# Optimization experiments

Hardware: AMD Instinct MI355X
Metric: run time of the kernel (lower is better)

The kernel has to match this reference:

```python
import jax, jax.numpy as jnp
from jax import lax
import numpy as np

# ---- geometry constants (from metadata / module __init__) ----
NA = 1152            # rotview (number of projection angles)
ND = 736             # det_count
NP = 512             # reconstructed image size
VOX = 1.0 / 0.7      # vox_scaling
D   = VOX * 595.0    # source-to-isocenter distance
DD  = VOX * 490.6    # isocenter-to-detector distance
DU  = VOX * 1.2858   # detector pixel spacing
DSD = D + DD         # source-to-detector distance
ANGLES = np.linspace(0.0, 2.0 * np.pi, NA, endpoint=False) + np.pi / 2.0

# ---- Shepp-Logan Fourier filter (skimage/torch-radon construction) ----
PAD = max(64, int(2 ** np.ceil(np.log2(2 * ND))))  # 2048

def _shepp_logan_filter(size):
    n = np.concatenate([np.arange(1, size // 2 + 1, 2),
                        np.arange(size // 2 - 1, 0, -2)])
    f = np.zeros(size)
    f[0] = 0.25
    f[1::2] = -1.0 / (np.pi * n) ** 2
    four = 2.0 * np.real(np.fft.fft(f))            # ramp filter
    omega = np.pi * np.fft.fftfreq(size)[1:]
    four[1:] *= np.sin(omega) / omega              # Shepp-Logan window
    return four[: size // 2 + 1].astype(np.float32)  # rfft half-spectrum

FILT = jnp.asarray(_shepp_logan_filter(PAD))
COS_A = jnp.asarray(np.cos(ANGLES).astype(np.float32))
SIN_A = jnp.asarray(np.sin(ANGLES).astype(np.float32))


def _filter_sinogram(sino):
    # sino: (NA, ND). Zero-pad to PAD, filter in Fourier domain, crop.
    padded = jnp.pad(sino, ((0, 0), (0, PAD - ND)))
    spec = jnp.fft.rfft(padded, axis=-1) * FILT
    filt = jnp.fft.irfft(spec, n=PAD, axis=-1)[:, :ND]
    return filt * (np.pi / (2.0 * NA))


def _backproject(filtered):
    # Pixel-driven fan-beam (flat detector) backprojection.
    c = (NP - 1) / 2.0
    coords = jnp.arange(NP, dtype=jnp.float32) - c
    ys, xs = jnp.meshgrid(coords, coords, indexing='ij')  # (NP, NP)

    def body(acc, inp):
        cb, sb, row = inp
        pdot = xs * cb + ys * sb            # pixel coord along source dir
        pe = -xs * sb + ys * cb             # pixel coord along detector axis
        den = D - pdot                      # source->pixel depth
        u = DSD * pe / den                  # detector coordinate (mm)
        iu = u / DU + (ND - 1) / 2.0        # fractional detector index
        i0 = jnp.floor(iu)
        frac = iu - i0
        i0i = i0.astype(jnp.int32)
        valid = (i0i >= 0) & (i0i < ND - 1) & (den > 0)
        i0c = jnp.clip(i0i, 0, ND - 2)
        v = row[i0c] * (1.0 - frac) + row[i0c + 1] * frac  # linear interp
        w = (D / den) ** 2                   # fan-beam distance weighting
        return acc + jnp.where(valid, w * v, 0.0), None

    img, _ = lax.scan(body, jnp.zeros((NP, NP), jnp.float32),
                      (COS_A, SIN_A, filtered))
    return img


def setup_inputs() -> dict:
    key = jax.random.key(0)
    x = jax.random.normal(key, (1, 1, NA, ND), dtype=jnp.float32)
    return {"x": x}


def reference(x):
    sino = x[0, 0]                          # (NA, ND) after squeeze
    filtered = _filter_sinogram(sino)
    fbp = _backproject(filtered)
    # mu -> HU -> normalize to [0, 1] window
    fbp_hu = (1000.0 * ((fbp - 0.0192) / 0.0192) - (-1024.0)) / (3072.0 - (-1024.0))
    return fbp_hu[None, None]               # (1, 1, 512, 512)
```

## Files before the change

kernel.cpp:

```cpp
#include <hip/hip_runtime.h>
#include <math.h>

#ifndef M_PI
#define M_PI 3.14159265358979323846
#endif

#define NAANG 1152
#define NDET  736
#define NPIX  512
#define PADN  2048
#define NHALF 1025

#define OFF_COST  0
#define OFF_FILTF 8192
#define OFF_H     12416
#define OFF_TRIG  20608
#define OFF_FS    39040
#define OFF_PART  3430528

typedef int int32x4_t __attribute__((ext_vector_type(4)));
__device__ float llvm_amdgcn_struct_buffer_load_fp32(int32x4_t srsrc,
                                                     int vindex, int voffset,
                                                     int soffset, int cachepolicy)
    __asm("llvm.amdgcn.struct.buffer.load.f32");

__global__ void costab_kernel(float* __restrict__ cosT) {
    int r = blockIdx.x * 256 + threadIdx.x;
    cosT[r] = (float)cos(2.0 * M_PI * (double)r / (double)PADN);
}

__global__ void filt_spec_kernel(const float* __restrict__ cosT,
                                 float* __restrict__ filt_f) {
    __shared__ float red[256];
    const int m = blockIdx.x;
    const int t = threadIdx.x;
    float s = 0.f;
    for (int j = t; j < 1024; j += 256) {
        int n = (j < 512) ? (2 * j + 1) : (2047 - 2 * j);
        float fj = (float)(-1.0 / ((M_PI * n) * (M_PI * n)));
        s += fj * cosT[(m * (2 * j + 1)) & (PADN - 1)];
    }
    red[t] = s;
    __syncthreads();
    for (int w = 128; w > 0; w >>= 1) {
        if (t < w) red[t] += red[t + w];
        __syncthreads();
    }
    if (t == 0) {
        double four = 2.0 * (0.25 + (double)red[0]);
        if (m > 0) {
            double om = M_PI * (double)m / (double)PADN;
            four *= sin(om) / om;
        }
        filt_f[m] = (float)four;
    }
}

__global__ void h_kernel(const float* __restrict__ cosT,
                         const float* __restrict__ filt_f,
                         float* __restrict__ h, float4* __restrict__ trig) {
    __shared__ float red[256];
    const int k = blockIdx.x;
    const int t = threadIdx.x;
    if (t == 0 && k < NAANG) {
        double ang = 2.0 * M_PI * (double)k / (double)NAANG + M_PI / 2.0;
        double c = cos(ang), s = sin(ang);
        double K = 1085.6 / 1.2858;
        trig[k] = make_float4((float)c, (float)s, (float)(K * c), (float)(K * s));
    }
    float s = 0.f;
    for (int m = t; m <= 1024; m += 256) {
        float F = filt_f[m];
        float c;
        if (m == 0) c = 1.f;
        else if (m == 1024) c = (k & 1) ? -1.f : 1.f;
        else c = 2.f * cosT[(m * k) & (PADN - 1)];
        s += F * c;
    }
    red[t] = s;
    __syncthreads();
    for (int w = 128; w > 0; w >>= 1) {
        if (t < w) red[t] += red[t + w];
        __syncthreads();
    }
    if (t == 0)
        h[k] = (float)((double)red[0] / (double)PADN * (M_PI / (2.0 * (double)NAANG)));
}

__global__ void conv_kernel(const float* __restrict__ x,
                            const float* __restrict__ h,
                            float* __restrict__ fs) {
    __shared__ float sh2[2816];
    __shared__ float srow[NDET];
    const int row = blockIdx.x;
    const int t = threadIdx.x;
    const float4* h4 = (const float4*)h;
    for (int i = t; i < 704; i += 192) ((float4*)sh2)[i] = h4[i & 511];
    const float4* x4 = (const float4*)(x + row * NDET);
    for (int i = t; i < NDET / 4; i += 192) ((float4*)srow)[i] = x4[i];
    __syncthreads();

    const int t4 = 4 * t;
    float o0 = 0.f, o1 = 0.f, o2 = 0.f, o3 = 0.f;
    #pragma unroll 2
    for (int j = 0; j < NDET; j += 4) {
        float4 r4 = *(const float4*)&srow[j];
        const int A = t4 + PADN - j;
        float4 hlo = *(const float4*)&sh2[A - 4];
        float4 hhi = *(const float4*)&sh2[A];
        o0 = fmaf(r4.x, hhi.x, o0); o0 = fmaf(r4.y, hlo.w, o0);
        o0 = fmaf(r4.z, hlo.z, o0); o0 = fmaf(r4.w, hlo.y, o0);
        o1 = fmaf(r4.x, hhi.y, o1); o1 = fmaf(r4.y, hhi.x, o1);
        o1 = fmaf(r4.z, hlo.w, o1); o1 = fmaf(r4.w, hlo.z, o1);
        o2 = fmaf(r4.x, hhi.z, o2); o2 = fmaf(r4.y, hhi.y, o2);
        o2 = fmaf(r4.z, hhi.x, o2); o2 = fmaf(r4.w, hlo.w, o2);
        o3 = fmaf(r4.x, hhi.w, o3); o3 = fmaf(r4.y, hhi.z, o3);
        o3 = fmaf(r4.z, hhi.y, o3); o3 = fmaf(r4.w, hhi.x, o3);
    }
    if (t < NDET / 4)
        *(float4*)&fs[row * NDET + t4] = make_float4(o0, o1, o2, o3);
}

#define GEO(AA, S)                                                       \
  {                                                                      \
    float4 q = trig[abase + (AA)];           \
    const float* rp_ = fs + (size_t)(abase + (AA)) * NDET;               \
    uintptr_t ua_ = (uintptr_t)rp_;                                      \
    int32x4_t sA_ = { (int)ua_, (int)(ua_ >> 32) | 0x00040000, 735,      \
                      0x00020000 };                                      \
    uintptr_t ub_ = ua_ + 4;                                             \
    int32x4_t sB_ = { (int)ub_, (int)(ub_ >> 32) | 0x00040000, 735,      \
                      0x00020000 };                                      \
    float den0 = fmaf(-xs, q.x, fmaf(-ys0, q.y, Dg));                    \
    float kpe0 = fmaf(ys0, q.z, -(xs * q.w));                            \
    float den1 = den0 - q.y, den2 = den1 - q.y, den3 = den2 - q.y;       \
    float kpe1 = kpe0 + q.z, kpe2 = kpe1 + q.z, kpe3 = kpe2 + q.z;       \
    float r0 = __builtin_amdgcn_rcpf(den0);                              \
    float r1 = __builtin_amdgcn_rcpf(den1);                              \
    float r2 = __builtin_amdgcn_rcpf(den2);                              \
    float r3 = __builtin_amdgcn_rcpf(den3);                              \
    float iu0 = fmaf(kpe0, r0, 367.5f);                                  \
    float iu1 = fmaf(kpe1, r1, 367.5f);                                  \
    float iu2 = fmaf(kpe2, r2, 367.5f);                                  \
    float iu3 = fmaf(kpe3, r3, 367.5f);                                  \
    int i0 = (int)floorf(iu0);                                           \
    int i1 = (int)floorf(iu1);                                           \
    int i2 = (int)floorf(iu2);                                           \
    int i3 = (int)floorf(iu3);                                           \
    asm("v_fract_f32 %0, %1" : "=v"(S##f0) : "v"(iu0));                  \
    asm("v_fract_f32 %0, %1" : "=v"(S##f1) : "v"(iu1));                  \
    asm("v_fract_f32 %0, %1" : "=v"(S##f2) : "v"(iu2));                  \
    asm("v_fract_f32 %0, %1" : "=v"(S##f3) : "v"(iu3));                  \
    S##g0l = llvm_amdgcn_struct_buffer_load_fp32(sA_, i0, 0, 0, 0);      \
    S##g0h = llvm_amdgcn_struct_buffer_load_fp32(sB_, i0, 0, 0, 0);      \
    S##g1l = llvm_amdgcn_struct_buffer_load_fp32(sA_, i1, 0, 0, 0);      \
    S##g1h = llvm_amdgcn_struct_buffer_load_fp32(sB_, i1, 0, 0, 0);      \
    S##g2l = llvm_amdgcn_struct_buffer_load_fp32(sA_, i2, 0, 0, 0);      \
    S##g2h = llvm_amdgcn_struct_buffer_load_fp32(sB_, i2, 0, 0, 0);      \
    S##g3l = llvm_amdgcn_struct_buffer_load_fp32(sA_, i3, 0, 0, 0);      \
    S##g3h = llvm_amdgcn_struct_buffer_load_fp32(sB_, i3, 0, 0, 0);      \
    S##w0 = r0 * r0; S##w1 = r1 * r1; S##w2 = r2 * r2; S##w3 = r3 * r3;  \
  }

#define CONSUME(S)                                                       \
  {                                                                      \
    float v0 = fmaf(S##f0, S##g0h - S##g0l, S##g0l);                     \
    float v1 = fmaf(S##f1, S##g1h - S##g1l, S##g1l);                     \
    float v2 = fmaf(S##f2, S##g2h - S##g2l, S##g2l);                     \
    float v3 = fmaf(S##f3, S##g3h - S##g3l, S##g3l);                     \
    acc0 = fmaf(S##w0, v0, acc0); acc1 = fmaf(S##w1, v1, acc1);          \
    acc2 = fmaf(S##w2, v2, acc2); acc3 = fmaf(S##w3, v3, acc3);          \
  }

#define DECLSET(S)                                                       \
    float S##g0l, S##g0h, S##g1l, S##g1h, S##g2l, S##g2h, S##g3l, S##g3h;\
    float S##f0, S##f1, S##f2, S##f3, S##w0, S##w1, S##w2, S##w3;

template<int NCH>
__global__ __launch_bounds__(256, 6)
void backproj_kernel(const float* __restrict__ fs,
                     const float4* __restrict__ trig,
                     float* __restrict__ partial) {
    constexpr int ACL = NAANG / NCH;
    static_assert(ACL % 3 == 0, "pipeline tail assumes ACL divisible by 3");
    const int t = threadIdx.x;
    const int abase = blockIdx.z * ACL;
    const int ix = blockIdx.x * 256 + t;
    const int iy = blockIdx.y * 4;
    const float xs  = (float)ix - 255.5f;
    const float ys0 = (float)iy - 255.5f;
    const float Dg = 850.0f;

    float acc0 = 0.f, acc1 = 0.f, acc2 = 0.f, acc3 = 0.f;
    DECLSET(A) DECLSET(B) DECLSET(C)

    GEO(0, A);
    GEO(1, B);
    int a = 0;
    for (; a + 5 < ACL; a += 3) {
        GEO(a + 2, C); CONSUME(A);
        GEO(a + 3, A); CONSUME(B);
        GEO(a + 4, B); CONSUME(C);
    }
    GEO(a + 2, C);
    CONSUME(A); CONSUME(B); CONSUME(C);

    float* outp = partial + ((size_t)blockIdx.z * NPIX + iy) * NPIX + ix;
    outp[0 * NPIX] = acc0;
    outp[1 * NPIX] = acc1;
    outp[2 * NPIX] = acc2;
    outp[3 * NPIX] = acc3;
}

template<int NCH>
__global__ void combine_kernel(const float* __restrict__ partial,
                               float* __restrict__ out) {
    int p = blockIdx.x * 256 + threadIdx.x;
    float s = 0.f;
    #pragma unroll
    for (int c = 0; c < NCH; ++c) s += partial[c * NPIX * NPIX + p];
    out[p] = fmaf(s, (float)(722500.0 * 1000.0 / 0.0192 / 4096.0), 0.005859375f);
}

extern "C" void kernel_launch(void* const* d_in, const int* in_sizes, int n_in,
                              void* d_out, int out_size, void* d_ws, size_t ws_size,
                              hipStream_t stream) {
    const float* x = (const float*)d_in[0];
    float* out = (float*)d_out;

    char* ws = (char*)d_ws;
    float*  cosT   = (float*)(ws + OFF_COST);
    float*  filt_f = (float*)(ws + OFF_FILTF);
    float*  h      = (float*)(ws + OFF_H);
    float4* trig   = (float4*)(ws + OFF_TRIG);
    float*  fs     = (float*)(ws + OFF_FS);
    float*  part   = (float*)(ws + OFF_PART);

    costab_kernel<<<PADN / 256, 256, 0, stream>>>(cosT);
    filt_spec_kernel<<<NHALF, 256, 0, stream>>>(cosT, filt_f);
    h_kernel<<<PADN, 256, 0, stream>>>(cosT, filt_f, h, trig);
    conv_kernel<<<NAANG, 192, 0, stream>>>(x, h, fs);

    const size_t pbytes = (size_t)NPIX * NPIX * 4;
    if (ws_size >= OFF_PART + 8 * pbytes) {
        backproj_kernel<8><<<dim3(2, 128, 8), 256, 0, stream>>>(fs, trig, part);
        combine_kernel<8><<<NPIX * NPIX / 256, 256, 0, stream>>>(part, out);
    } else if (ws_size >= OFF_PART + 4 * pbytes) {
        backproj_kernel<4><<<dim3(2, 128, 4), 256, 0, stream>>>(fs, trig, part);
        combine_kernel<4><<<NPIX * NPIX / 256, 256, 0, stream>>>(part, out);
    } else if (ws_size >= OFF_PART + 2 * pbytes) {
        backproj_kernel<2><<<dim3(2, 128, 2), 256, 0, stream>>>(fs, trig, part);
        combine_kernel<2><<<NPIX * NPIX / 256, 256, 0, stream>>>(part, out);
    } else {
        backproj_kernel<1><<<dim3(2, 128, 1), 256, 0, stream>>>(fs, trig, part);
        combine_kernel<1><<<NPIX * NPIX / 256, 256, 0, stream>>>(part, out);
    }
}
```

Baseline: 248.1 us.

## Fetch interpolation pairs with single 2-wide buffer loads and shorten pipeline

Replaces the two scalar buffer loads per detector sample (two descriptors offset by one element) with a single 8-byte buffer load that returns both neighbours, halving the number of gather instructions. Out-of-range handling moves from descriptor bounds to an explicit zeroing of the weight when the index reaches the last detector. The software pipeline depth drops from three sets of in-flight loads to two, and the occupancy hint rises from 6 to 8 waves to compensate with more resident wavefronts. There is a risk of unaligned 8-byte loads and less latency hiding per wave.

After: 262.8 us. 5.9% more time.

```diff
diff --git a/kernel.cpp b/kernel.cpp
--- a/kernel.cpp
+++ b/kernel.cpp
@@ -19,10 +19,11 @@
 #define OFF_PART  3430528
 
 typedef int int32x4_t __attribute__((ext_vector_type(4)));
-__device__ float llvm_amdgcn_struct_buffer_load_fp32(int32x4_t srsrc,
-                                                     int vindex, int voffset,
-                                                     int soffset, int cachepolicy)
-    __asm("llvm.amdgcn.struct.buffer.load.f32");
+typedef float f32x2 __attribute__((ext_vector_type(2)));
+__device__ f32x2 llvm_amdgcn_struct_buffer_load_2xfp32(int32x4_t srsrc,
+                                                       int vindex, int voffset,
+                                                       int soffset, int cachepolicy)
+    __asm("llvm.amdgcn.struct.buffer.load.v2f32");
 
 __global__ void costab_kernel(float* __restrict__ cosT) {
     int r = blockIdx.x * 256 + threadIdx.x;
@@ -126,10 +127,7 @@
     float4 q = trig[abase + (AA)];           \
     const float* rp_ = fs + (size_t)(abase + (AA)) * NDET;               \
     uintptr_t ua_ = (uintptr_t)rp_;                                      \
-    int32x4_t sA_ = { (int)ua_, (int)(ua_ >> 32) | 0x00040000, 735,      \
-                      0x00020000 };                                      \
-    uintptr_t ub_ = ua_ + 4;                                             \
-    int32x4_t sB_ = { (int)ub_, (int)(ub_ >> 32) | 0x00040000, 735,      \
+    int32x4_t sA_ = { (int)ua_, (int)(ua_ >> 32) | 0x00040000, 736,      \
                       0x00020000 };                                      \
     float den0 = fmaf(-xs, q.x, fmaf(-ys0, q.y, Dg));                    \
     float kpe0 = fmaf(ys0, q.z, -(xs * q.w));                            \
@@ -151,38 +149,37 @@
     asm("v_fract_f32 %0, %1" : "=v"(S##f1) : "v"(iu1));                  \
     asm("v_fract_f32 %0, %1" : "=v"(S##f2) : "v"(iu2));                  \
     asm("v_fract_f32 %0, %1" : "=v"(S##f3) : "v"(iu3));                  \
-    S##g0l = llvm_amdgcn_struct_buffer_load_fp32(sA_, i0, 0, 0, 0);      \
-    S##g0h = llvm_amdgcn_struct_buffer_load_fp32(sB_, i0, 0, 0, 0);      \
-    S##g1l = llvm_amdgcn_struct_buffer_load_fp32(sA_, i1, 0, 0, 0);      \
-    S##g1h = llvm_amdgcn_struct_buffer_load_fp32(sB_, i1, 0, 0, 0);      \
-    S##g2l = llvm_amdgcn_struct_buffer_load_fp32(sA_, i2, 0, 0, 0);      \
-    S##g2h = llvm_amdgcn_struct_buffer_load_fp32(sB_, i2, 0, 0, 0);      \
-    S##g3l = llvm_amdgcn_struct_buffer_load_fp32(sA_, i3, 0, 0, 0);      \
-    S##g3h = llvm_amdgcn_struct_buffer_load_fp32(sB_, i3, 0, 0, 0);      \
-    S##w0 = r0 * r0; S##w1 = r1 * r1; S##w2 = r2 * r2; S##w3 = r3 * r3;  \
+    S##g0 = llvm_amdgcn_struct_buffer_load_2xfp32(sA_, i0, 0, 0, 0);     \
+    S##g1 = llvm_amdgcn_struct_buffer_load_2xfp32(sA_, i1, 0, 0, 0);     \
+    S##g2 = llvm_amdgcn_struct_buffer_load_2xfp32(sA_, i2, 0, 0, 0);     \
+    S##g3 = llvm_amdgcn_struct_buffer_load_2xfp32(sA_, i3, 0, 0, 0);     \
+    float w0_ = r0 * r0, w1_ = r1 * r1, w2_ = r2 * r2, w3_ = r3 * r3;    \
+    S##w0 = (iu0 < 735.0f) ? w0_ : 0.f;                                  \
+    S##w1 = (iu1 < 735.0f) ? w1_ : 0.f;                                  \
+    S##w2 = (iu2 < 735.0f) ? w2_ : 0.f;                                  \
+    S##w3 = (iu3 < 735.0f) ? w3_ : 0.f;                                  \
   }
 
 #define CONSUME(S)                                                       \
   {                                                                      \
-    float v0 = fmaf(S##f0, S##g0h - S##g0l, S##g0l);                     \
-    float v1 = fmaf(S##f1, S##g1h - S##g1l, S##g1l);                     \
-    float v2 = fmaf(S##f2, S##g2h - S##g2l, S##g2l);                     \
-    float v3 = fmaf(S##f3, S##g3h - S##g3l, S##g3l);                     \
+    float v0 = fmaf(S##f0, S##g0.y - S##g0.x, S##g0.x);                  \
+    float v1 = fmaf(S##f1, S##g1.y - S##g1.x, S##g1.x);                  \
+    float v2 = fmaf(S##f2, S##g2.y - S##g2.x, S##g2.x);                  \
+    float v3 = fmaf(S##f3, S##g3.y - S##g3.x, S##g3.x);                  \
     acc0 = fmaf(S##w0, v0, acc0); acc1 = fmaf(S##w1, v1, acc1);          \
     acc2 = fmaf(S##w2, v2, acc2); acc3 = fmaf(S##w3, v3, acc3);          \
   }
 
 #define DECLSET(S)                                                       \
-    float S##g0l, S##g0h, S##g1l, S##g1h, S##g2l, S##g2h, S##g3l, S##g3h;\
+    f32x2 S##g0, S##g1, S##g2, S##g3;                                    \
     float S##f0, S##f1, S##f2, S##f3, S##w0, S##w1, S##w2, S##w3;
 
 template<int NCH>
-__global__ __launch_bounds__(256, 6)
+__global__ __launch_bounds__(256, 8)
 void backproj_kernel(const float* __restrict__ fs,
                      const float4* __restrict__ trig,
                      float* __restrict__ partial) {
     constexpr int ACL = NAANG / NCH;
-    static_assert(ACL % 3 == 0, "pipeline tail assumes ACL divisible by 3");
     const int t = threadIdx.x;
     const int abase = blockIdx.z * ACL;
     const int ix = blockIdx.x * 256 + t;
@@ -192,18 +189,16 @@
     const float Dg = 850.0f;
 
     float acc0 = 0.f, acc1 = 0.f, acc2 = 0.f, acc3 = 0.f;
-    DECLSET(A) DECLSET(B) DECLSET(C)
+    DECLSET(A) DECLSET(B)
 
     GEO(0, A);
-    GEO(1, B);
     int a = 0;
-    for (; a + 5 < ACL; a += 3) {
-        GEO(a + 2, C); CONSUME(A);
-        GEO(a + 3, A); CONSUME(B);
-        GEO(a + 4, B); CONSUME(C);
-    }
-    GEO(a + 2, C);
-    CONSUME(A); CONSUME(B); CONSUME(C);
+    for (; a + 2 < ACL; a += 2) {
+        GEO(a + 1, B); CONSUME(A);
+        GEO(a + 2, A); CONSUME(B);
+    }
+    GEO(ACL - 1, B);
+    CONSUME(A); CONSUME(B);
 
     float* outp = partial + ((size_t)blockIdx.z * NPIX + iy) * NPIX + ix;
     outp[0 * NPIX] = acc0;
```
